# Kernel optimization log

Hardware: AMD Instinct MI355X
Metric: run time of the kernel (lower is better)

Reference implementation:

```python
import jax, jax.numpy as jnp
import numpy as np


def _depthwise3x3(x_nhwc, w):
    # w: (3, 3, 1, C) — depthwise conv, padding=1, matches torch Conv2d(groups=C)
    return jax.lax.conv_general_dilated(
        x_nhwc, w, window_strides=(1, 1), padding='SAME',
        dimension_numbers=('NHWC', 'HWIO', 'NHWC'),
        feature_group_count=x_nhwc.shape[-1])


def _stripe_attn(q, k, v, lepe_w, B, H, W, nh, hd, ss, axis, scale):
    # q/k/v: (B, H, W, nh*hd); axis 0 = horizontal stripes, 1 = vertical
    pad_h = (-H) % ss if axis == 0 else 0
    pad_w = (-W) % ss if axis == 1 else 0
    if pad_h or pad_w:
        pad = ((0, 0), (0, pad_h), (0, pad_w), (0, 0))
        q, k, v = jnp.pad(q, pad), jnp.pad(k, pad), jnp.pad(v, pad)
    Hp, Wp = q.shape[1], q.shape[2]
    lepe = _depthwise3x3(v, lepe_w)  # (B, Hp, Wp, nh*hd)

    if axis == 0:
        nS = Hp // ss
        def to_win(t):  # -> (B*nS*Wp, nh, ss, hd)
            t = t.reshape(B, nS, ss, Wp, nh, hd)
            return t.transpose(0, 1, 3, 4, 2, 5).reshape(B * nS * Wp, nh, ss, hd)
    else:
        nS = Wp // ss
        def to_win(t):  # -> (B*Hp*nS, nh, ss, hd)
            t = t.reshape(B, Hp, nS, ss, nh, hd)
            return t.transpose(0, 1, 2, 4, 3, 5).reshape(B * Hp * nS, nh, ss, hd)

    qw, kw, vw, lw = to_win(q), to_win(k), to_win(v), to_win(lepe)
    attn = jax.nn.softmax(jnp.einsum('wnqd,wnkd->wnqk', qw, kw) / scale, axis=-1)
    out = jnp.einsum('wnqk,wnkd->wnqd', attn, vw) + lw  # (Wnum, nh, ss, hd)

    if axis == 0:
        out = out.transpose(0, 2, 1, 3).reshape(B, nS, Wp, ss, nh * hd)
        out = out.transpose(0, 1, 3, 2, 4).reshape(B, Hp, Wp, nh * hd)
    else:
        out = out.transpose(0, 2, 1, 3).reshape(B, Hp, nS, ss, nh * hd)
        out = out.reshape(B, Hp, Wp, nh * hd)
    return out[:, :H, :W, :].reshape(B, H * W, nh * hd)


def setup_inputs() -> dict:
    key = jax.random.key(0)
    ks = jax.random.split(key, 6)
    B, H, W, dim, n_heads, ss = 8, 64, 64, 512, 16, 8
    half = dim // 2
    x = jax.random.normal(ks[0], (B, H * W, dim), dtype=jnp.float32)
    w_qkv = jax.random.normal(ks[1], (3 * dim, dim), dtype=jnp.float32) * 0.02
    w_proj = jax.random.normal(ks[2], (dim, dim), dtype=jnp.float32) * 0.02
    b_proj = jnp.zeros((dim,), dtype=jnp.float32)
    lepe_h_w = jax.random.normal(ks[3], (3, 3, 1, half), dtype=jnp.float32) * 0.1
    lepe_v_w = jax.random.normal(ks[4], (3, 3, 1, half), dtype=jnp.float32) * 0.1
    return {"x": x, "w_qkv": w_qkv, "w_proj": w_proj, "b_proj": b_proj,
            "lepe_h_w": lepe_h_w, "lepe_v_w": lepe_v_w, "H": H, "W": W}


def reference(x, w_qkv, w_proj, b_proj, lepe_h_w, lepe_v_w, H, W):
    B, L, C = x.shape
    n_heads, ss = 16, 8
    hd = C // n_heads
    scale = float(np.sqrt(hd))
    qkv = x @ w_qkv.T  # (B, L, 3C)
    q, k, v = jnp.split(qkv, 3, axis=-1)
    q = q.reshape(B, H, W, C)
    k = k.reshape(B, H, W, C)
    v = v.reshape(B, H, W, C)
    half = C // 2
    nh_h = n_heads // 2
    nh_v = n_heads - nh_h
    out_h = _stripe_attn(q[..., :half], k[..., :half], v[..., :half],
                         lepe_h_w, B, H, W, nh_h, hd, ss, axis=0, scale=scale)
    out_v = _stripe_attn(q[..., half:], k[..., half:], v[..., half:],
                         lepe_v_w, B, H, W, nh_v, hd, ss, axis=1, scale=scale)
    out = jnp.concatenate([out_h, out_v], axis=-1)
    return out @ w_proj.T + b_proj
```

## Files before the change

### kernel.cpp

```cpp
#include <hip/hip_runtime.h>
#include <hip/hip_bf16.h>
#include <stdint.h>

typedef _Float16 half2v __attribute__((ext_vector_type(2)));
typedef _Float16 half8v __attribute__((ext_vector_type(8)));
typedef uint32_t u32x4  __attribute__((ext_vector_type(4)));
typedef float    f32x4  __attribute__((ext_vector_type(4)));

__device__ __forceinline__ unsigned short f2h(float f) {
  _Float16 h = (_Float16)f;
  return __builtin_bit_cast(unsigned short, h);
}
__device__ __forceinline__ half2v bch2(uint32_t u) {
  return __builtin_bit_cast(half2v, u);
}
__device__ __forceinline__ uint32_t pkrtz_u32(float a, float b) {
  return __builtin_bit_cast(uint32_t, __builtin_amdgcn_cvt_pkrtz(a, b));
}

__device__ __forceinline__ int qkv_idx(int half, int b, int n, int h, int w) {
  int idx = half * 8388608 + (b * 8 + n) * 131072;
  idx += (half == 0) ? ((h >> 3) * 16384 + w * 256 + (h & 7) * 32)
                     : (h * 2048 + w * 32);
  return idx;
}

#define GLOAD_LDS16(gsrc, lbase)                                          \
  __builtin_amdgcn_global_load_lds(                                       \
      (const __attribute__((address_space(1))) uint32_t*)(gsrc),          \
      (__attribute__((address_space(3))) uint32_t*)(lbase), 16, 0, 0)

__global__ __launch_bounds__(256) void cvt_f32_f16(const float* __restrict__ in,
                                                   unsigned short* __restrict__ out,
                                                   int n4) {
  int i = blockIdx.x * 256 + threadIdx.x;
  if (i >= n4) return;
  float4 f = reinterpret_cast<const float4*>(in)[i];
  ushort4 u;
  u.x = f2h(f.x); u.y = f2h(f.y); u.z = f2h(f.z); u.w = f2h(f.w);
  reinterpret_cast<ushort4*>(out)[i] = u;
}

__global__ __launch_bounds__(256) void gemm_qkv(
    const float* __restrict__ X,
    const unsigned short* __restrict__ B,
    unsigned short* __restrict__ Cq)
{
  constexpr int K = 512, N = 1536;
  __shared__ float          Af[2][128 * 32];
  __shared__ unsigned short Bh[2][128 * 32];
  const int tid  = threadIdx.x;
  const int gn   = N >> 7;
  const int cpx  = gridDim.x >> 3;
  const int bid  = blockIdx.x;
  const int wgid = (bid & 7) * cpx + (bid >> 3);
  const int m0   = (wgid / gn) * 128;
  const int n0   = (wgid % gn) * 128;
  const int wave = tid >> 6, lane = tid & 63;
  const int wr = wave >> 1, wc = wave & 1;
  const int sr  = tid >> 2;
  const int scB = ((tid & 3) ^ ((tid >> 3) & 3)) * 8;
  const size_t bBase0 = (size_t)(n0 + sr) * K + scB;
  const size_t bBase1 = (size_t)(n0 + 64 + sr) * K + scB;
  const int arow = tid >> 3;
  const int acsw = ((tid & 7) ^ (arow & 7)) * 4;
  const size_t aBase = (size_t)(m0 + arow) * K + acsw;
  char* ldsA = (char*)(&Af[0][0]) + (tid & ~63) * 16;
  char* ldsB = (char*)(&Bh[0][0]) + (tid & ~63) * 16;

#define STAGE_Q(bsel, kt)                                                \
  do {                                                                   \
    GLOAD_LDS16(X + aBase + (kt),            ldsA + (bsel) * 16384);     \
    GLOAD_LDS16(X + aBase + 32 * K + (kt),   ldsA + (bsel) * 16384 + 4096); \
    GLOAD_LDS16(X + aBase + 64 * K + (kt),   ldsA + (bsel) * 16384 + 8192); \
    GLOAD_LDS16(X + aBase + 96 * K + (kt),   ldsA + (bsel) * 16384 + 12288);\
    GLOAD_LDS16(B + bBase0 + (kt),           ldsB + (bsel) * 8192);      \
    GLOAD_LDS16(B + bBase1 + (kt),           ldsB + (bsel) * 8192 + 4096);  \
  } while (0)

  STAGE_Q(0, 0);

  f32x4 acc[4][4];
  const f32x4 zero = {0.f, 0.f, 0.f, 0.f};
  #pragma unroll
  for (int i = 0; i < 4; ++i)
    #pragma unroll
    for (int j = 0; j < 4; ++j) acc[i][j] = zero;

  const int lr    = lane & 15;
  const int kg    = lane >> 4;
  const int slotB = kg ^ ((lr >> 1) & 3);
  const int pA0   = (2 * kg)     ^ (lr & 7);
  const int pA1   = (2 * kg + 1) ^ (lr & 7);

  auto compute = [&](const float* Asb, const unsigned short* Bsb) {
    half8v bfr[4], af[4];
    #pragma unroll
    for (int j = 0; j < 4; ++j)
      bfr[j] = *reinterpret_cast<const half8v*>(Bsb + (wc * 64 + j * 16 + lr) * 32 + slotB * 8);
    #pragma unroll
    for (int i = 0; i < 4; ++i) {
      const float* rowp = Asb + (wr * 64 + i * 16 + lr) * 32;
      const float4 fa = *reinterpret_cast<const float4*>(rowp + pA0 * 4);
      const float4 fb = *reinterpret_cast<const float4*>(rowp + pA1 * 4);
      u32x4 pk;
      pk[0] = pkrtz_u32(fa.x, fa.y);
      pk[1] = pkrtz_u32(fa.z, fa.w);
      pk[2] = pkrtz_u32(fb.x, fb.y);
      pk[3] = pkrtz_u32(fb.z, fb.w);
      af[i] = __builtin_bit_cast(half8v, pk);
    }
    __builtin_amdgcn_s_setprio(1);
    #pragma unroll
    for (int i = 0; i < 4; ++i)
      #pragma unroll
      for (int j = 0; j < 4; ++j)
        acc[i][j] = __builtin_amdgcn_mfma_f32_16x16x32_f16(bfr[j], af[i], acc[i][j], 0, 0, 0);
    __builtin_amdgcn_s_setprio(0);
  };

  const int nt = K >> 5;
  for (int t = 0; t < nt - 1; ++t) {
    STAGE_Q((t + 1) & 1, (t + 1) * 32);
    asm volatile("s_waitcnt vmcnt(6)" ::: "memory");
    __builtin_amdgcn_s_barrier();
    __builtin_amdgcn_sched_barrier(0);
    compute(&Af[t & 1][0], &Bh[t & 1][0]);
    __builtin_amdgcn_s_barrier();
    __builtin_amdgcn_sched_barrier(0);
  }
  asm volatile("s_waitcnt vmcnt(0)" ::: "memory");
  __builtin_amdgcn_s_barrier();
  __builtin_amdgcn_sched_barrier(0);
  compute(&Af[(nt - 1) & 1][0], &Bh[(nt - 1) & 1][0]);
#undef STAGE_Q

  const int cr = (lane >> 4) * 4;
  const int cc = lane & 15;
  const int mb   = m0 + wr * 64;
  const int btok = mb >> 12;
  const int htok = (mb >> 6) & 63;
  #pragma unroll
  for (int j = 0; j < 4; ++j) {
    const int nb    = n0 + wc * 64 + j * 16 + cr;
    const int tq    = nb >> 9;
    const int halfc = (nb >> 8) & 1;
    const int nn    = (nb & 255) >> 5;
    const int ch4   = nb & 31;
    int base = tq * 16777216 + halfc * 8388608 + (btok * 8 + nn) * 131072 + ch4;
    base += halfc ? (htok * 2048) : ((htok >> 3) * 16384 + (htok & 7) * 32);
    const int wstride = halfc ? 32 : 256;
    #pragma unroll
    for (int i = 0; i < 4; ++i) {
      const int wpix = i * 16 + cc;
      uint2 r;
      r.x = pkrtz_u32(acc[i][j][0], acc[i][j][1]);
      r.y = pkrtz_u32(acc[i][j][2], acc[i][j][3]);
      *reinterpret_cast<uint2*>(Cq + base + wpix * wstride) = r;
    }
  }
}

__global__ __launch_bounds__(256) void gemm_proj(
    const unsigned short* __restrict__ A,
    const unsigned short* __restrict__ B,
    float* __restrict__ Cf,
    const float* __restrict__ bias)
{
  constexpr int K = 512, N = 512;
  __shared__ unsigned short As[2][128 * 32];
  __shared__ unsigned short Bs[2][128 * 32];
  const int tid  = threadIdx.x;
  const int gn   = N >> 7;
  const int cpx  = gridDim.x >> 3;
  const int bid  = blockIdx.x;
  const int wgid = (bid & 7) * cpx + (bid >> 3);
  const int m0   = (wgid / gn) * 128;
  const int n0   = (wgid % gn) * 128;
  const int wave = tid >> 6, lane = tid & 63;
  const int wr = wave >> 1, wc = wave & 1;
  const int sr = tid >> 2;
  const int sc = ((tid & 3) ^ ((tid >> 3) & 3)) * 8;
  const size_t aBase0 = (size_t)(m0 + sr) * K + sc;
  const size_t aBase1 = (size_t)(m0 + 64 + sr) * K + sc;
  const size_t bBase0 = (size_t)(n0 + sr) * K + sc;
  const size_t bBase1 = (size_t)(n0 + 64 + sr) * K + sc;
  char* ldsA = (char*)(&As[0][0]) + (tid & ~63) * 16;
  char* ldsB = (char*)(&Bs[0][0]) + (tid & ~63) * 16;

#define STAGE_P(bsel, kofs)                                        \
  do {                                                             \
    GLOAD_LDS16(A + aBase0 + (kofs), ldsA + (bsel) * 8192);        \
    GLOAD_LDS16(A + aBase1 + (kofs), ldsA + (bsel) * 8192 + 4096); \
    GLOAD_LDS16(B + bBase0 + (kofs), ldsB + (bsel) * 8192);        \
    GLOAD_LDS16(B + bBase1 + (kofs), ldsB + (bsel) * 8192 + 4096); \
  } while (0)

  STAGE_P(0, 0);

  f32x4 acc[4][4];
  const f32x4 zero = {0.f, 0.f, 0.f, 0.f};
  #pragma unroll
  for (int i = 0; i < 4; ++i)
    #pragma unroll
    for (int j = 0; j < 4; ++j) acc[i][j] = zero;

  const int lr   = lane & 15;
  const int slot = (lane >> 4) ^ ((lr >> 1) & 3);

  auto compute = [&](const unsigned short* Asb, const unsigned short* Bsb) {
    half8v af[4], bfr[4];
    #pragma unroll
    for (int i = 0; i < 4; ++i)
      af[i] = *reinterpret_cast<const half8v*>(Asb + (wr * 64 + i * 16 + lr) * 32 + slot * 8);
    #pragma unroll
    for (int j = 0; j < 4; ++j)
      bfr[j] = *reinterpret_cast<const half8v*>(Bsb + (wc * 64 + j * 16 + lr) * 32 + slot * 8);
    __builtin_amdgcn_s_setprio(1);
    #pragma unroll
    for (int i = 0; i < 4; ++i)
      #pragma unroll
      for (int j = 0; j < 4; ++j)
        acc[i][j] = __builtin_amdgcn_mfma_f32_16x16x32_f16(bfr[j], af[i], acc[i][j], 0, 0, 0);
    __builtin_amdgcn_s_setprio(0);
  };

  const int nt = K >> 5;
  for (int t = 0; t < nt - 1; ++t) {
    STAGE_P((t + 1) & 1, (t + 1) * 32);
    asm volatile("s_waitcnt vmcnt(4)" ::: "memory");
    __builtin_amdgcn_s_barrier();
    __builtin_amdgcn_sched_barrier(0);
    compute(&As[t & 1][0], &Bs[t & 1][0]);
    __builtin_amdgcn_s_barrier();
    __builtin_amdgcn_sched_barrier(0);
  }
  asm volatile("s_waitcnt vmcnt(0)" ::: "memory");
  __builtin_amdgcn_s_barrier();
  __builtin_amdgcn_sched_barrier(0);
  compute(&As[(nt - 1) & 1][0], &Bs[(nt - 1) & 1][0]);
#undef STAGE_P

  const int cr = (lane >> 4) * 4;
  const int cc = lane & 15;
  #pragma unroll
  for (int j = 0; j < 4; ++j) {
    const int n = n0 + wc * 64 + j * 16 + cr;
    const float4 b4 = *reinterpret_cast<const float4*>(bias + n);
    #pragma unroll
    for (int i = 0; i < 4; ++i) {
      const int m = m0 + wr * 64 + i * 16 + cc;
      float4 r;
      r.x = acc[i][j][0] + b4.x;
      r.y = acc[i][j][1] + b4.y;
      r.z = acc[i][j][2] + b4.z;
      r.w = acc[i][j][3] + b4.w;
      *reinterpret_cast<float4*>(Cf + (size_t)m * N + n) = r;
    }
  }
}

__global__ __launch_bounds__(256) void attn_lepe(
    const unsigned short* __restrict__ qkvp,
    const unsigned short* __restrict__ wlep,
    unsigned short* __restrict__ outp)
{
  const int gw   = (int)((blockIdx.x * 256 + threadIdx.x) >> 6);
  const int lane = threadIdx.x & 63;
  const int half = gw >> 14;
  const int id   = gw & 16383;
  const int b    = id >> 11;
  const int n    = (id >> 8) & 7;
  int h0, w0;
  if (half == 0) { h0 = ((id >> 5) & 7) * 8; w0 = (id & 31) * 2; }
  else           { h0 = ((id >> 3) & 31) * 2; w0 = (id & 7) * 8; }
  const int baseA = qkv_idx(half, b, n, h0, w0);
  const int dWin  = (half == 0) ? 256 : 2048;
  const int baseB = baseA + dWin;

  const int qr = lane >> 3, kr = lane & 7;
  const unsigned short* qA = qkvp + baseA + qr * 32;
  const unsigned short* kA = qkvp + 16777216 + baseA + kr * 32;
  float sA = 0.f, sB = 0.f;
  #pragma unroll
  for (int c = 0; c < 4; ++c) {
    const u32x4 qa = *reinterpret_cast<const u32x4*>(qA + c * 8);
    const u32x4 ka = *reinterpret_cast<const u32x4*>(kA + c * 8);
    const u32x4 qb = *reinterpret_cast<const u32x4*>(qA + dWin + c * 8);
    const u32x4 kb = *reinterpret_cast<const u32x4*>(kA + dWin + c * 8);
    #pragma unroll
    for (int e = 0; e < 4; ++e) {
      sA = __builtin_amdgcn_fdot2(bch2(qa[e]), bch2(ka[e]), sA, false);
      sB = __builtin_amdgcn_fdot2(bch2(qb[e]), bch2(kb[e]), sB, false);
    }
  }
  const float scl = 0.17677669529663687f;
  const float pA = __expf(sA * scl);
  const float pB = __expf(sB * scl);
  float denA = pA, denB = pB;
  denA += __shfl_xor(denA, 1); denA += __shfl_xor(denA, 2); denA += __shfl_xor(denA, 4);
  denB += __shfl_xor(denB, 1); denB += __shfl_xor(denB, 2); denB += __shfl_xor(denB, 4);
  const float aAv = pA * __builtin_amdgcn_rcpf(denA);
  const float aBv = pB * __builtin_amdgcn_rcpf(denB);
  const uint32_t adu = pkrtz_u32(aAv, aBv);

  const int dgrp = lane & 3;
  const int win  = (lane >> 2) & 1;
  const int qr2  = lane >> 3;
  const int d0   = dgrp * 8;
  const int mybase = win ? baseB : baseA;
  const unsigned short* vwin = qkvp + 33554432 + mybase;

  half2v o01 = {0,0}, o23 = {0,0}, o45 = {0,0}, o67 = {0,0};
  #pragma unroll
  for (int k = 0; k < 8; ++k) {
    const uint32_t pairw = (uint32_t)__shfl((int)adu, qr2 * 8 + k);
    const half2v ph = bch2(pairw);
    const _Float16 av = win ? ph.y : ph.x;
    const half2v ak2 = {av, av};
    const u32x4 vv = *reinterpret_cast<const u32x4*>(vwin + k * 32 + d0);
    o01 += ak2 * bch2(vv[0]);
    o23 += ak2 * bch2(vv[1]);
    o45 += ak2 * bch2(vv[2]);
    o67 += ak2 * bch2(vv[3]);
  }

  const int hq = (half == 0) ? (h0 + qr2) : (h0 + win);
  const int wq = (half == 0) ? (w0 + win) : (w0 + qr2);
  const unsigned short* vplane = qkvp + 33554432;
  const unsigned short* wl = wlep + half * 2304 + n * 32 + d0;
  half2v l01 = {0,0}, l23 = {0,0}, l45 = {0,0}, l67 = {0,0};
  #pragma unroll
  for (int dy = -1; dy <= 1; ++dy) {
    #pragma unroll
    for (int dx = -1; dx <= 1; ++dx) {
      const int hh = hq + dy, ww = wq + dx;
      u32x4 vv = {0u, 0u, 0u, 0u};
      if ((unsigned)hh < 64u && (unsigned)ww < 64u)
        vv = *reinterpret_cast<const u32x4*>(vplane + qkv_idx(half, b, n, hh, ww) + d0);
      const u32x4 wt = *reinterpret_cast<const u32x4*>(wl + ((dy + 1) * 3 + dx + 1) * 256);
      l01 += bch2(wt[0]) * bch2(vv[0]);
      l23 += bch2(wt[1]) * bch2(vv[1]);
      l45 += bch2(wt[2]) * bch2(vv[2]);
      l67 += bch2(wt[3]) * bch2(vv[3]);
    }
  }

  const int m = b * 4096 + hq * 64 + wq;
  const int chan0 = half * 256 + n * 32;
  u32x4 r;
  r[0] = __builtin_bit_cast(uint32_t, (half2v)(o01 + l01));
  r[1] = __builtin_bit_cast(uint32_t, (half2v)(o23 + l23));
  r[2] = __builtin_bit_cast(uint32_t, (half2v)(o45 + l45));
  r[3] = __builtin_bit_cast(uint32_t, (half2v)(o67 + l67));
  *reinterpret_cast<u32x4*>(outp + (size_t)m * 512 + chan0 + d0) = r;
}

extern "C" void kernel_launch(void* const* d_in, const int* in_sizes, int n_in,
                              void* d_out, int out_size, void* d_ws, size_t ws_size,
                              hipStream_t stream) {
  const float* x      = (const float*)d_in[0];
  const float* w_qkv  = (const float*)d_in[1];
  const float* w_proj = (const float*)d_in[2];
  const float* b_proj = (const float*)d_in[3];
  const float* lepe_h = (const float*)d_in[4];
  const float* lepe_v = (const float*)d_in[5];
  float* out = (float*)d_out;

  char* ws = (char*)d_ws;
  unsigned short* qkv_p   = (unsigned short*)ws;
  unsigned short* ah      = (unsigned short*)(ws + 100663296);
  unsigned short* wqkv_h  = (unsigned short*)(ws + 134217728);
  unsigned short* wproj_h = (unsigned short*)(ws + 135790592);
  unsigned short* wlep_h  = (unsigned short*)(ws + 136314880);

  cvt_f32_f16<<<768, 256, 0, stream>>>(w_qkv, wqkv_h, 196608);
  cvt_f32_f16<<<256, 256, 0, stream>>>(w_proj, wproj_h, 65536);
  cvt_f32_f16<<<3,   256, 0, stream>>>(lepe_h, wlep_h, 576);
  cvt_f32_f16<<<3,   256, 0, stream>>>(lepe_v, wlep_h + 2304, 576);

  gemm_qkv<<<3072, 256, 0, stream>>>(x, wqkv_h, qkv_p);

  attn_lepe<<<8192, 256, 0, stream>>>(qkv_p, wlep_h, ah);

  gemm_proj<<<1024, 256, 0, stream>>>(ah, wproj_h, out, b_proj);
}
```

Before: 187.0 us.

## Stage QKV GEMM A-tile via registers with fp16 conversion before LDS

```diff
diff --git a/kernel.cpp b/kernel.cpp
--- a/kernel.cpp
+++ b/kernel.cpp
@@ -47,7 +47,7 @@
     unsigned short* __restrict__ Cq)
 {
   constexpr int K = 512, N = 1536;
-  __shared__ float          Af[2][128 * 32];
+  __shared__ unsigned short Ah[2][128 * 32];
   __shared__ unsigned short Bh[2][128 * 32];
   const int tid  = threadIdx.x;
   const int gn   = N >> 7;
@@ -58,27 +58,43 @@
   const int n0   = (wgid % gn) * 128;
   const int wave = tid >> 6, lane = tid & 63;
   const int wr = wave >> 1, wc = wave & 1;
-  const int sr  = tid >> 2;
-  const int scB = ((tid & 3) ^ ((tid >> 3) & 3)) * 8;
-  const size_t bBase0 = (size_t)(n0 + sr) * K + scB;
-  const size_t bBase1 = (size_t)(n0 + 64 + sr) * K + scB;
-  const int arow = tid >> 3;
-  const int acsw = ((tid & 7) ^ (arow & 7)) * 4;
-  const size_t aBase = (size_t)(m0 + arow) * K + acsw;
-  char* ldsA = (char*)(&Af[0][0]) + (tid & ~63) * 16;
+  const int sr = tid >> 2;
+  const int sc = ((tid & 3) ^ ((tid >> 3) & 3)) * 8;
+  const size_t aBase0 = (size_t)(m0 + sr) * K + sc;
+  const size_t aBase1 = (size_t)(m0 + 64 + sr) * K + sc;
+  const size_t bBase0 = (size_t)(n0 + sr) * K + sc;
+  const size_t bBase1 = (size_t)(n0 + 64 + sr) * K + sc;
   char* ldsB = (char*)(&Bh[0][0]) + (tid & ~63) * 16;
 
-#define STAGE_Q(bsel, kt)                                                \
-  do {                                                                   \
-    GLOAD_LDS16(X + aBase + (kt),            ldsA + (bsel) * 16384);     \
-    GLOAD_LDS16(X + aBase + 32 * K + (kt),   ldsA + (bsel) * 16384 + 4096); \
-    GLOAD_LDS16(X + aBase + 64 * K + (kt),   ldsA + (bsel) * 16384 + 8192); \
-    GLOAD_LDS16(X + aBase + 96 * K + (kt),   ldsA + (bsel) * 16384 + 12288);\
-    GLOAD_LDS16(B + bBase0 + (kt),           ldsB + (bsel) * 8192);      \
-    GLOAD_LDS16(B + bBase1 + (kt),           ldsB + (bsel) * 8192 + 4096);  \
+  float4 a00, a01, a10, a11;
+
+#define LOADA(kt)                                                         \
+  do {                                                                    \
+    a00 = *reinterpret_cast<const float4*>(X + aBase0 + (kt));            \
+    a01 = *reinterpret_cast<const float4*>(X + aBase0 + (kt) + 4);        \
+    a10 = *reinterpret_cast<const float4*>(X + aBase1 + (kt));            \
+    a11 = *reinterpret_cast<const float4*>(X + aBase1 + (kt) + 4);        \
   } while (0)
 
-  STAGE_Q(0, 0);
+#define GLOADB(bsel, kt)                                                  \
+  do {                                                                    \
+    GLOAD_LDS16(B + bBase0 + (kt), ldsB + (bsel) * 8192);                 \
+    GLOAD_LDS16(B + bBase1 + (kt), ldsB + (bsel) * 8192 + 4096);          \
+  } while (0)
+
+#define WRITEA(abuf)                                                      \
+  do {                                                                    \
+    u32x4 w0, w1;                                                         \
+    w0[0] = pkrtz_u32(a00.x, a00.y); w0[1] = pkrtz_u32(a00.z, a00.w);     \
+    w0[2] = pkrtz_u32(a01.x, a01.y); w0[3] = pkrtz_u32(a01.z, a01.w);     \
+    w1[0] = pkrtz_u32(a10.x, a10.y); w1[1] = pkrtz_u32(a10.z, a10.w);     \
+    w1[2] = pkrtz_u32(a11.x, a11.y); w1[3] = pkrtz_u32(a11.z, a11.w);     \
+    *reinterpret_cast<u32x4*>((abuf) + tid * 8)        = w0;              \
+    *reinterpret_cast<u32x4*>((abuf) + tid * 8 + 2048) = w1;              \
+  } while (0)
+
+  LOADA(0);
+  GLOADB(0, 0);
 
   f32x4 acc[4][4];
   const f32x4 zero = {0.f, 0.f, 0.f, 0.f};
@@ -87,29 +103,17 @@
     #pragma unroll
     for (int j = 0; j < 4; ++j) acc[i][j] = zero;
 
-  const int lr    = lane & 15;
-  const int kg    = lane >> 4;
-  const int slotB = kg ^ ((lr >> 1) & 3);
-  const int pA0   = (2 * kg)     ^ (lr & 7);
-  const int pA1   = (2 * kg + 1) ^ (lr & 7);
-
-  auto compute = [&](const float* Asb, const unsigned short* Bsb) {
-    half8v bfr[4], af[4];
+  const int lr   = lane & 15;
+  const int slot = (lane >> 4) ^ ((lr >> 1) & 3);
+
+  auto compute = [&](const unsigned short* Asb, const unsigned short* Bsb) {
+    half8v af[4], bfr[4];
+    #pragma unroll
+    for (int i = 0; i < 4; ++i)
+      af[i] = *reinterpret_cast<const half8v*>(Asb + (wr * 64 + i * 16 + lr) * 32 + slot * 8);
     #pragma unroll
     for (int j = 0; j < 4; ++j)
-      bfr[j] = *reinterpret_cast<const half8v*>(Bsb + (wc * 64 + j * 16 + lr) * 32 + slotB * 8);
-    #pragma unroll
-    for (int i = 0; i < 4; ++i) {
-      const float* rowp = Asb + (wr * 64 + i * 16 + lr) * 32;
-      const float4 fa = *reinterpret_cast<const float4*>(rowp + pA0 * 4);
-      const float4 fb = *reinterpret_cast<const float4*>(rowp + pA1 * 4);
-      u32x4 pk;
-      pk[0] = pkrtz_u32(fa.x, fa.y);
-      pk[1] = pkrtz_u32(fa.z, fa.w);
-      pk[2] = pkrtz_u32(fb.x, fb.y);
-      pk[3] = pkrtz_u32(fb.z, fb.w);
-      af[i] = __builtin_bit_cast(half8v, pk);
-    }
+      bfr[j] = *reinterpret_cast<const half8v*>(Bsb + (wc * 64 + j * 16 + lr) * 32 + slot * 8);
     __builtin_amdgcn_s_setprio(1);
     #pragma unroll
     for (int i = 0; i < 4; ++i)
@@ -120,20 +124,28 @@
   };
 
   const int nt = K >> 5;
-  for (int t = 0; t < nt - 1; ++t) {
-    STAGE_Q((t + 1) & 1, (t + 1) * 32);
-    asm volatile("s_waitcnt vmcnt(6)" ::: "memory");
+  for (int t = 0; t < nt; ++t) {
+    unsigned short* abuf = (t & 1) ? &Ah[1][0] : &Ah[0][0];
+    const unsigned short* bbuf = (t & 1) ? &Bh[1][0] : &Bh[0][0];
+    asm volatile("s_waitcnt vmcnt(2)" ::: "memory");
+    WRITEA(abuf);
+    if (t + 1 < nt) {
+      LOADA((t + 1) * 32);
+      GLOADB((t + 1) & 1, (t + 1) * 32);
+      asm volatile("s_waitcnt vmcnt(6)" ::: "memory");
+    } else {
+      asm volatile("s_waitcnt vmcnt(0)" ::: "memory");
+    }
+    asm volatile("s_waitcnt lgkmcnt(0)" ::: "memory");
     __builtin_amdgcn_s_barrier();
     __builtin_amdgcn_sched_barrier(0);
-    compute(&Af[t & 1][0], &Bh[t & 1][0]);
+    compute(abuf, bbuf);
     __builtin_amdgcn_s_barrier();
     __builtin_amdgcn_sched_barrier(0);
   }
-  asm volatile("s_waitcnt vmcnt(0)" ::: "memory");
-  __builtin_amdgcn_s_barrier();
-  __builtin_amdgcn_sched_barrier(0);
-  compute(&Af[(nt - 1) & 1][0], &Bh[(nt - 1) & 1][0]);
-#undef STAGE_Q
+#undef LOADA
+#undef GLOADB
+#undef WRITEA
 
   const int cr = (lane >> 4) * 4;
   const int cc = lane & 15;
```

Result: no change. 185.6 us (-0.7%).
